# Kernel optimization log

Measured on AMD Instinct MI355X. Metric: run time of the kernel, lower is better.

Reference implementation:

```python
import jax, jax.numpy as jnp
import numpy as np


def gcn_conv(h, edge_index, num_nodes):
    # Symmetric-normalized GCN aggregation: out[i] = sum_{(j->i)} h[j] / sqrt(deg(i)*deg(j))
    row, col = edge_index[0], edge_index[1]
    deg = jax.ops.segment_sum(jnp.ones(col.shape, dtype=h.dtype), col, num_segments=num_nodes)
    d_inv_sqrt = jnp.where(deg > 0, jax.lax.rsqrt(jnp.maximum(deg, 1.0)), 0.0)
    w = d_inv_sqrt[row] * d_inv_sqrt[col]           # [E]
    msg = h[row] * w[:, None]                        # [E, D] gather + scale
    return jax.ops.segment_sum(msg, col, num_segments=num_nodes)  # [N, D] scatter-add


def setup_inputs() -> dict:
    key = jax.random.key(0)
    k1, k2, k3, k4 = jax.random.split(key, 4)
    N, E, F_IN, F_HID, F_OUT = 100000, 1600000, 128, 64, 40
    x = jax.random.normal(k1, (N, F_IN), dtype=jnp.float32)
    edge_index = jax.random.randint(k2, (2, E), 0, N, dtype=jnp.int64)
    # xavier_uniform with gain=1.414 (as in reset_parameters); biases zero
    def xavier(k, shape, gain=1.414):
        fan_out, fan_in = shape
        a = gain * np.sqrt(6.0 / (fan_in + fan_out))
        return jax.random.uniform(k, shape, jnp.float32, -a, a)
    W1 = xavier(k3, (F_HID, F_IN))
    b1 = jnp.zeros((F_HID,), dtype=jnp.float32)
    W2 = xavier(k4, (F_OUT, F_HID))
    b2 = jnp.zeros((F_OUT,), dtype=jnp.float32)
    return {"x": x, "edge_index": edge_index, "W1": W1, "b1": b1, "W2": W2, "b2": b2}


def reference(x, edge_index, W1, b1, W2, b2):
    # GNN.forward with num_layers=2, use_mp=True, eval mode (dropout inactive)
    N = x.shape[0]
    h = x @ W1.T                      # [N, nhid]
    h = gcn_conv(h, edge_index, N)
    h = jax.nn.relu(h + b1)
    h = h @ W2.T                      # [N, nclass]
    h = gcn_conv(h, edge_index, N)
    return h + b2
```

## Files before the change

kernel.cpp:

```cpp
#include <hip/hip_runtime.h>
#include <hip/hip_fp16.h>


typedef __attribute__((ext_vector_type(8))) _Float16 half8v;
typedef __attribute__((ext_vector_type(4))) float   float4v;

__device__ __forceinline__ void binfill_body(char* smem, const int* __restrict__ ed,
                                             int* __restrict__ gbincnt,
                                             unsigned* __restrict__ binbuf,
                                             int E, int cap, int bid) {
  int*            hist   = (int*)smem;
  int*            cursor = hist + 512;
  unsigned*       rec    = (unsigned*)(cursor + 512);
  unsigned short* binv   = (unsigned short*)(rec + 4096);
  int*            s_is64 = (int*)(binv + 4096);
  int t = threadIdx.x;
  hist[t] = 0; hist[t + 256] = 0;
  if (t == 0) *s_is64 = 1;
  __syncthreads();
  {
    int any = 0;
    #pragma unroll
    for (int u = 0; u < 8; ++u) {
      int idx = 2 * (t * 8 + u) + 1;
      if (idx < 2 * E && ed[idx] != 0) any = 1;
    }
    if (any) *s_is64 = 0;
  }
  __syncthreads();
  const int is64 = *s_is64;
  const int base = bid * 4096;
  const int nE = min(4096, E - base);
  for (int j = t; j < nE; j += 256) {
    int e = base + j;
    int r = is64 ? ed[2 * e] : ed[e];
    int c = is64 ? ed[2 * (E + e)] : ed[E + e];
    rec[j] = (unsigned)r | ((unsigned)(c & 255) << 17);
    binv[j] = (unsigned short)(c >> 8);
    atomicAdd(&hist[c >> 8], 1);
  }
  __syncthreads();
  for (int b = t; b < 512; b += 256) {
    int h = hist[b];
    cursor[b] = h ? atomicAdd(&gbincnt[b], h) : 0;
  }
  __syncthreads();
  for (int j = t; j < nE; j += 256) {
    int bin = binv[j];
    int pos = atomicAdd(&cursor[bin], 1);
    if (pos < cap)
      binbuf[(size_t)bin * cap + pos] = rec[j];
  }
}

__device__ __forceinline__ void gemm1_body(char* smem, const float* __restrict__ X,
                                           const float* __restrict__ W,
                                           unsigned char* __restrict__ h1q,
                                           float* __restrict__ sc1, int N, int bid) {
  _Float16* wl = (_Float16*)smem;
  const int t = threadIdx.x;
  const int row0 = bid * 128;
  const int w = t >> 6, l = t & 63;
  const int m0 = w * 32;
  const int lr = l & 15, q = l >> 4;

  float4 xr[4][2][2];
  #pragma unroll
  for (int kc = 0; kc < 4; ++kc) {
    #pragma unroll
    for (int mt = 0; mt < 2; ++mt) {
      int row = min(row0 + m0 + mt * 16 + lr, N - 1);
      const float* p = &X[(size_t)row * 128 + kc * 32 + q * 8];
      xr[kc][mt][0] = *(const float4*)p;
      xr[kc][mt][1] = *(const float4*)(p + 4);
    }
  }

  #pragma unroll
  for (int j = 0; j < 8; ++j) {
    int qq = t + 256 * j;
    int r = qq >> 5, k4 = qq & 31;
    float4 v = *(const float4*)&W[(size_t)r * 128 + k4 * 4];
    _Float16 h4[4] = {(_Float16)v.x, (_Float16)v.y, (_Float16)v.z, (_Float16)v.w};
    int k = (k4 * 4) ^ ((r & 7) * 8);
    *(float2*)&wl[r * 128 + k] = *(float2*)h4;
  }
  __syncthreads();

  float4v acc[2][4] = {};
  #pragma unroll
  for (int kc = 0; kc < 4; ++kc) {
    half8v a[2], b[4];
    #pragma unroll
    for (int mt = 0; mt < 2; ++mt) {
      float4 v0 = xr[kc][mt][0], v1 = xr[kc][mt][1];
      _Float16 h8[8] = {(_Float16)v0.x, (_Float16)v0.y, (_Float16)v0.z, (_Float16)v0.w,
                        (_Float16)v1.x, (_Float16)v1.y, (_Float16)v1.z, (_Float16)v1.w};
      a[mt] = *(half8v*)h8;
    }
    #pragma unroll
    for (int nt = 0; nt < 4; ++nt) {
      int n = nt * 16 + lr;
      int k = (kc * 32 + q * 8) ^ ((n & 7) * 8);
      b[nt] = *(half8v*)&wl[n * 128 + k];
    }
    #pragma unroll
    for (int mt = 0; mt < 2; ++mt)
      #pragma unroll
      for (int nt = 0; nt < 4; ++nt)
        acc[mt][nt] = __builtin_amdgcn_mfma_f32_16x16x32_f16(a[mt], b[nt], acc[mt][nt], 0, 0, 0);
  }

  #pragma unroll
  for (int mt = 0; mt < 2; ++mt) {
    #pragma unroll
    for (int r = 0; r < 4; ++r) {
      int row = row0 + m0 + mt * 16 + q * 4 + r;
      if (row < N) {
        float v0 = acc[mt][0][r];
        float v1 = acc[mt][1][r];
        float v2 = acc[mt][2][r];
        float v3 = acc[mt][3][r];
        float m = fmaxf(fmaxf(fabsf(v0), fabsf(v1)), fmaxf(fabsf(v2), fabsf(v3)));
        #pragma unroll
        for (int off = 1; off < 16; off <<= 1)
          m = fmaxf(m, __shfl_xor(m, off));
        float inv = (m > 0.f) ? (127.f / m) : 0.f;
        unsigned char* dst = h1q + (size_t)row * 64;
        int q0 = (int)rintf(v0 * inv);
        int q1 = (int)rintf(v1 * inv);
        int q2 = (int)rintf(v2 * inv);
        int q3 = (int)rintf(v3 * inv);
        q0 = max(-127, min(127, q0));
        q1 = max(-127, min(127, q1));
        q2 = max(-127, min(127, q2));
        q3 = max(-127, min(127, q3));
        dst[lr]      = (unsigned char)(signed char)q0;
        dst[lr + 16] = (unsigned char)(signed char)q1;
        dst[lr + 32] = (unsigned char)(signed char)q2;
        dst[lr + 48] = (unsigned char)(signed char)q3;
        if (lr == 0) sc1[row] = m * (1.f / 127.f);
      }
    }
  }
}

__launch_bounds__(256)
__global__ void k_prep(const int* __restrict__ ed, int* __restrict__ gbincnt,
                       unsigned* __restrict__ binbuf, int E, int cap,
                       const float* __restrict__ X, const float* __restrict__ W,
                       unsigned char* __restrict__ h1q, float* __restrict__ sc1,
                       int N, int FB) {
  __shared__ __align__(16) char smem[28680];
  if (blockIdx.x < FB)
    binfill_body(smem, ed, gbincnt, binbuf, E, cap, blockIdx.x);
  else
    gemm1_body(smem, X, W, h1q, sc1, N, blockIdx.x - FB);
}

__global__ void k_degscat(const unsigned* __restrict__ binbuf, const int* __restrict__ gbincnt,
                          float* __restrict__ dis, int* __restrict__ rowptr,
                          int* __restrict__ srcs, float* __restrict__ sc1,
                          int NBINS, int N, int cap) {
  __shared__ int sd[512];
  __shared__ int cnt[256];
  __shared__ int sc[256];
  __shared__ int bc[256][8];
  __shared__ unsigned rec[8192];
  int t = threadIdx.x, b = blockIdx.x;
  sd[t]       = (t < NBINS)       ? min(gbincnt[t], cap)       : 0;
  sd[t + 256] = (t + 256 < NBINS) ? min(gbincnt[t + 256], cap) : 0;
  cnt[t] = 0;
  #pragma unroll
  for (int k = 0; k < 8; ++k) bc[t][k] = 0;
  __syncthreads();
  for (int off = 1; off < 512; off <<= 1) {
    int v0 = (t >= off) ? sd[t - off] : 0;
    int v1 = sd[t + 256 - off];
    __syncthreads();
    sd[t] += v0; sd[t + 256] += v1;
    __syncthreads();
  }
  const int mybase = (b == 0) ? 0 : sd[b - 1];
  if (b == NBINS - 1 && t == 0) rowptr[N] = sd[NBINS - 1];

  int n = min(gbincnt[b], cap);
  const unsigned* buf = binbuf + (size_t)b * cap;
  for (int j = t; j < n; j += 256) {
    unsigned v = buf[j];
    rec[j] = v;
    atomicAdd(&cnt[v >> 17], 1);
    atomicAdd(&bc[v >> 17][(v & 0x1FFFF) >> 14], 1);
  }
  __syncthreads();
  sc[t] = cnt[t];
  __syncthreads();
  for (int off = 1; off < 256; off <<= 1) {
    int v = (t >= off) ? sc[t - off] : 0;
    __syncthreads();
    sc[t] += v;
    __syncthreads();
  }
  int rp = mybase + ((t == 0) ? 0 : sc[t - 1]);
  int node = b * 256 + t;
  if (node < N) {
    int d = cnt[t];
    float dv = (d > 0) ? rsqrtf((float)d) : 0.f;
    dis[node] = dv;
    rowptr[node] = rp;
    sc1[node] *= dv;
  }
  {
    int base2 = rp;
    #pragma unroll
    for (int k = 0; k < 8; ++k) {
      int c = bc[t][k];
      bc[t][k] = base2;
      base2 += c;
    }
  }
  __syncthreads();
  for (int j = t; j < n; j += 256) {
    unsigned v = rec[j];
    int pos = atomicAdd(&bc[v >> 17][(v & 0x1FFFF) >> 14], 1);
    srcs[pos] = (int)(v & 0x1FFFF);
  }
}

__launch_bounds__(256)
__global__ void k_gemm2_mfma(const __half* __restrict__ Xh, const float* __restrict__ W,
                             const float* __restrict__ dis, unsigned char* __restrict__ h2,
                             int N) {
  __shared__ _Float16 xl[128 * 64];
  __shared__ _Float16 wl[48 * 64];
  const int t = threadIdx.x;
  const int row0 = blockIdx.x * 128;

  for (int i = t; i < 48 * 8; i += 256) {
    int c = i >> 3, kq = i & 7;
    _Float16 h8[8];
    #pragma unroll
    for (int j = 0; j < 8; ++j)
      h8[j] = (c < 40) ? (_Float16)W[c * 64 + kq * 8 + j] : (_Float16)0.f;
    *(float4*)&wl[c * 64 + ((kq * 8) ^ ((c & 7) * 8))] = *(float4*)h8;
  }
  for (int i = t; i < 1024; i += 256) {
    int r = i >> 3, kq = i & 7;
    int row = row0 + r;
    float4 v = make_float4(0.f, 0.f, 0.f, 0.f);
    if (row < N) v = *(const float4*)&Xh[(size_t)row * 64 + kq * 8];
    *(float4*)&xl[r * 64 + ((kq * 8) ^ ((r & 7) * 8))] = v;
  }
  __syncthreads();

  const int w = t >> 6, l = t & 63;
  const int m0 = w * 32;
  const int lr = l & 15, q = l >> 4;

  float4v acc[2][3] = {};
  #pragma unroll
  for (int kc = 0; kc < 2; ++kc) {
    half8v a[2], b[3];
    #pragma unroll
    for (int mt = 0; mt < 2; ++mt) {
      int m = m0 + mt * 16 + lr;
      int k = (kc * 32 + q * 8) ^ ((m & 7) * 8);
      a[mt] = *(half8v*)&xl[m * 64 + k];
    }
    #pragma unroll
    for (int nt = 0; nt < 3; ++nt) {
      int n = nt * 16 + lr;
      int k = (kc * 32 + q * 8) ^ ((n & 7) * 8);
      b[nt] = *(half8v*)&wl[n * 64 + k];
    }
    #pragma unroll
    for (int mt = 0; mt < 2; ++mt)
      #pragma unroll
      for (int nt = 0; nt < 3; ++nt)
        acc[mt][nt] = __builtin_amdgcn_mfma_f32_16x16x32_f16(a[mt], b[nt], acc[mt][nt], 0, 0, 0);
  }

  #pragma unroll
  for (int mt = 0; mt < 2; ++mt) {
    #pragma unroll
    for (int r = 0; r < 4; ++r) {
      int row = row0 + m0 + mt * 16 + q * 4 + r;
      if (row < N) {
        float dr = dis[row];
        float v0 = acc[mt][0][r] * dr;
        float v1 = acc[mt][1][r] * dr;
        float v2 = acc[mt][2][r] * dr;
        float m = fmaxf(fabsf(v0), fmaxf(fabsf(v1), fabsf(v2)));
        #pragma unroll
        for (int off = 1; off < 16; off <<= 1)
          m = fmaxf(m, __shfl_xor(m, off));
        float s = m * (1.f / 127.f);
        float inv = (m > 0.f) ? (127.f / m) : 0.f;
        unsigned char* dst = h2 + (size_t)row * 64;
        int q0 = (int)rintf(v0 * inv);
        int q1 = (int)rintf(v1 * inv);
        int q2 = (int)rintf(v2 * inv);
        q0 = max(-127, min(127, q0));
        q1 = max(-127, min(127, q1));
        q2 = max(-127, min(127, q2));
        dst[lr]      = (unsigned char)(signed char)q0;
        dst[lr + 16] = (unsigned char)(signed char)q1;
        if (lr + 32 < 40) dst[lr + 32] = (unsigned char)(signed char)q2;
        if (lr == 0) *(float*)&dst[40] = s;
        if (lr >= 1 && lr <= 5) *(int*)&dst[40 + 4 * lr] = 0;
      }
    }
  }
}

__launch_bounds__(256)
__global__ void k_conv64(const unsigned char* __restrict__ H, const float* __restrict__ sc1,
                         const int* __restrict__ rowptr, const int* __restrict__ srcs,
                         const float* __restrict__ dis, const float* __restrict__ b1,
                         __half* __restrict__ out, int N) {
  int t = threadIdx.x;
  int li = t & 7;
  int node = blockIdx.x * 32 + (t >> 3);
  if (node >= N) return;
  int s = rowptr[node], e = rowptr[node + 1];
  int last = e - 1;
  float a0 = 0.f, a1 = 0.f, a2 = 0.f, a3 = 0.f,
        a4 = 0.f, a5 = 0.f, a6 = 0.f, a7 = 0.f;
  for (int p = s; p < e; p += 8) {
    int sv[8]; uint2 rv[8]; float cv[8];
    #pragma unroll
    for (int u = 0; u < 8; ++u) sv[u] = srcs[min(p + u, last)];
    #pragma unroll
    for (int u = 0; u < 8; ++u) rv[u] = *(const uint2*)&H[(size_t)sv[u] * 64 + 8 * li];
    #pragma unroll
    for (int u = 0; u < 8; ++u) cv[u] = sc1[sv[u]];
    #pragma unroll
    for (int u = 0; u < 8; ++u) {
      if (p + u < e) {
        int x0 = (int)rv[u].x, x1 = (int)rv[u].y;
        float c = cv[u];
        a0 = fmaf((float)((x0 << 24) >> 24), c, a0);
        a1 = fmaf((float)((x0 << 16) >> 24), c, a1);
        a2 = fmaf((float)((x0 << 8)  >> 24), c, a2);
        a3 = fmaf((float)( x0        >> 24), c, a3);
        a4 = fmaf((float)((x1 << 24) >> 24), c, a4);
        a5 = fmaf((float)((x1 << 16) >> 24), c, a5);
        a6 = fmaf((float)((x1 << 8)  >> 24), c, a6);
        a7 = fmaf((float)( x1        >> 24), c, a7);
      }
    }
  }
  float dn = dis[node];
  const float* bb = b1 + 8 * li;
  __half hv[8];
  hv[0] = __float2half_rn(fmaxf(fmaf(a0, dn, bb[0]), 0.f));
  hv[1] = __float2half_rn(fmaxf(fmaf(a1, dn, bb[1]), 0.f));
  hv[2] = __float2half_rn(fmaxf(fmaf(a2, dn, bb[2]), 0.f));
  hv[3] = __float2half_rn(fmaxf(fmaf(a3, dn, bb[3]), 0.f));
  hv[4] = __float2half_rn(fmaxf(fmaf(a4, dn, bb[4]), 0.f));
  hv[5] = __float2half_rn(fmaxf(fmaf(a5, dn, bb[5]), 0.f));
  hv[6] = __float2half_rn(fmaxf(fmaf(a6, dn, bb[6]), 0.f));
  hv[7] = __float2half_rn(fmaxf(fmaf(a7, dn, bb[7]), 0.f));
  *(float4*)&out[(size_t)node * 64 + 8 * li] = *(float4*)hv;
}

__launch_bounds__(256)
__global__ void k_conv40(const unsigned char* __restrict__ H, const int* __restrict__ rowptr,
                         const int* __restrict__ srcs, const float* __restrict__ dis,
                         const float* __restrict__ b2, float* __restrict__ out, int N) {
  int t = threadIdx.x;
  int li = t & 7;
  int node = blockIdx.x * 32 + (t >> 3);
  if (node >= N) return;
  bool act = li < 5;
  int s = rowptr[node], e = rowptr[node + 1];
  int last = e - 1;
  float a0 = 0.f, a1 = 0.f, a2 = 0.f, a3 = 0.f,
        a4 = 0.f, a5 = 0.f, a6 = 0.f, a7 = 0.f;
  for (int p = s; p < e; p += 8) {
    int sv[8];
    #pragma unroll
    for (int u = 0; u < 8; ++u) sv[u] = srcs[min(p + u, last)];
    if (act) {
      uint2 rv[8]; float cv[8];
      #pragma unroll
      for (int u = 0; u < 8; ++u)
        rv[u] = *(const uint2*)&H[(size_t)sv[u] * 64 + 8 * li];
      #pragma unroll
      for (int u = 0; u < 8; ++u)
        cv[u] = *(const float*)&H[(size_t)sv[u] * 64 + 40];
      #pragma unroll
      for (int u = 0; u < 8; ++u) {
        if (p + u < e) {
          int x0 = (int)rv[u].x, x1 = (int)rv[u].y;
          float c = cv[u];
          a0 = fmaf((float)((x0 << 24) >> 24), c, a0);
          a1 = fmaf((float)((x0 << 16) >> 24), c, a1);
          a2 = fmaf((float)((x0 << 8)  >> 24), c, a2);
          a3 = fmaf((float)( x0        >> 24), c, a3);
          a4 = fmaf((float)((x1 << 24) >> 24), c, a4);
          a5 = fmaf((float)((x1 << 16) >> 24), c, a5);
          a6 = fmaf((float)((x1 << 8)  >> 24), c, a6);
          a7 = fmaf((float)( x1        >> 24), c, a7);
        }
      }
    }
  }
  if (act) {
    float dn = dis[node];
    const float* bb = b2 + 8 * li;
    float4 v0 = make_float4(fmaf(a0, dn, bb[0]), fmaf(a1, dn, bb[1]),
                            fmaf(a2, dn, bb[2]), fmaf(a3, dn, bb[3]));
    float4 v1 = make_float4(fmaf(a4, dn, bb[4]), fmaf(a5, dn, bb[5]),
                            fmaf(a6, dn, bb[6]), fmaf(a7, dn, bb[7]));
    *(float4*)&out[(size_t)node * 40 + 8 * li] = v0;
    *(float4*)&out[(size_t)node * 40 + 8 * li + 4] = v1;
  }
}

extern "C" void kernel_launch(void* const* d_in, const int* in_sizes, int n_in,
                              void* d_out, int out_size, void* d_ws, size_t ws_size,
                              hipStream_t stream) {
  const float* x  = (const float*)d_in[0];
  const int*   ed = (const int*)d_in[1];
  const float* W1 = (const float*)d_in[2];
  const float* b1 = (const float*)d_in[3];
  const float* W2 = (const float*)d_in[4];
  const float* b2 = (const float*)d_in[5];
  float* out = (float*)d_out;

  const int FIN = 128, FH = 64;
  const int N = in_sizes[0] / FIN;
  const int E = in_sizes[1] / 2;
  const int NBINS = (N + 255) >> 8;
  const int cap = 8192;

  char* ws = (char*)d_ws;
  size_t off = 0;
  auto alloc = [&](size_t bytes) {
    void* p = ws + off;
    off = (off + bytes + 255) & ~(size_t)255;
    return p;
  };
  int*           gbincnt = (int*)alloc(512 * 4);
  float*         dis     = (float*)alloc((size_t)N * 4);
  int*           rowptr  = (int*)alloc(((size_t)N + 1) * 4);
  int*           srcs    = (int*)alloc((size_t)E * 4);
  unsigned*      binbuf  = (unsigned*)alloc((size_t)NBINS * cap * 4);
  unsigned char* h1q     = (unsigned char*)alloc((size_t)N * 64);
  float*         sc1     = (float*)alloc((size_t)N * 4);
  __half*        h1b     = (__half*)alloc((size_t)N * FH * 2);
  unsigned char* h2      = (unsigned char*)alloc((size_t)N * 64);

  hipMemsetAsync(gbincnt, 0, 512 * 4, stream);

  int fb = (E + 4095) / 4096;
  int mb = (N + 127) / 128;
  int cb = (N + 31) / 32;
  k_prep<<<fb + mb, 256, 0, stream>>>(ed, gbincnt, binbuf, E, cap, x, W1, h1q, sc1, N, fb);
  k_degscat<<<NBINS, 256, 0, stream>>>(binbuf, gbincnt, dis, rowptr, srcs, sc1,
                                       NBINS, N, cap);
  k_conv64<<<cb, 256, 0, stream>>>(h1q, sc1, rowptr, srcs, dis, b1, h1b, N);
  k_gemm2_mfma<<<mb, 256, 0, stream>>>(h1b, W2, dis, h2, N);
  k_conv40<<<cb, 256, 0, stream>>>(h2, rowptr, srcs, dis, b2, out, N);
}
```

Before: 210.6 us.

## Fuse first-layer aggregation with second GEMM and halve binning chunk size

The layer-1 aggregation kernel and the layer-2 MFMA GEMM are merged into one kernel. Each block aggregates 32 nodes, writes the ReLU'd fp16 rows into LDS and multiplies them by W2 in place, so the fp16 intermediate h1b no longer goes through global memory and one launch disappears. Edge binning now uses 2048-edge chunks instead of 4096, with smaller shared memory, to get more blocks and more occupancy. Risks: only half the waves do MFMA work, every block reloads W2, and the smaller k_prep shared buffer must still be big enough for the GEMM1 path.

```diff
diff --git a/kernel.cpp b/kernel.cpp
--- a/kernel.cpp
+++ b/kernel.cpp
@@ -12,8 +12,8 @@
   int*            hist   = (int*)smem;
   int*            cursor = hist + 512;
   unsigned*       rec    = (unsigned*)(cursor + 512);
-  unsigned short* binv   = (unsigned short*)(rec + 4096);
-  int*            s_is64 = (int*)(binv + 4096);
+  unsigned short* binv   = (unsigned short*)(rec + 2048);
+  int*            s_is64 = (int*)(binv + 2048);
   int t = threadIdx.x;
   hist[t] = 0; hist[t + 256] = 0;
   if (t == 0) *s_is64 = 1;
@@ -29,8 +29,8 @@
   }
   __syncthreads();
   const int is64 = *s_is64;
-  const int base = bid * 4096;
-  const int nE = min(4096, E - base);
+  const int base = bid * 2048;
+  const int nE = min(2048, E - base);
   for (int j = t; j < nE; j += 256) {
     int e = base + j;
     int r = is64 ? ed[2 * e] : ed[e];
@@ -151,7 +151,7 @@
                        const float* __restrict__ X, const float* __restrict__ W,
                        unsigned char* __restrict__ h1q, float* __restrict__ sc1,
                        int N, int FB) {
-  __shared__ __align__(16) char smem[28680];
+  __shared__ __align__(16) char smem[16512];
   if (blockIdx.x < FB)
     binfill_body(smem, ed, gbincnt, binbuf, E, cap, blockIdx.x);
   else
@@ -228,68 +228,101 @@
 }
 
 __launch_bounds__(256)
-__global__ void k_gemm2_mfma(const __half* __restrict__ Xh, const float* __restrict__ W,
-                             const float* __restrict__ dis, unsigned char* __restrict__ h2,
-                             int N) {
-  __shared__ _Float16 xl[128 * 64];
+__global__ void k_conv64g2(const unsigned char* __restrict__ H, const float* __restrict__ sc1,
+                           const int* __restrict__ rowptr, const int* __restrict__ srcs,
+                           const float* __restrict__ dis, const float* __restrict__ b1,
+                           const float* __restrict__ W2, unsigned char* __restrict__ h2,
+                           int N) {
+  __shared__ _Float16 xl[32 * 64];
   __shared__ _Float16 wl[48 * 64];
-  const int t = threadIdx.x;
-  const int row0 = blockIdx.x * 128;
+  int t = threadIdx.x;
 
   for (int i = t; i < 48 * 8; i += 256) {
     int c = i >> 3, kq = i & 7;
-    _Float16 h8[8];
+    _Float16 h8w[8];
     #pragma unroll
     for (int j = 0; j < 8; ++j)
-      h8[j] = (c < 40) ? (_Float16)W[c * 64 + kq * 8 + j] : (_Float16)0.f;
-    *(float4*)&wl[c * 64 + ((kq * 8) ^ ((c & 7) * 8))] = *(float4*)h8;
-  }
-  for (int i = t; i < 1024; i += 256) {
-    int r = i >> 3, kq = i & 7;
-    int row = row0 + r;
-    float4 v = make_float4(0.f, 0.f, 0.f, 0.f);
-    if (row < N) v = *(const float4*)&Xh[(size_t)row * 64 + kq * 8];
-    *(float4*)&xl[r * 64 + ((kq * 8) ^ ((r & 7) * 8))] = v;
-  }
-  __syncthreads();
-
-  const int w = t >> 6, l = t & 63;
-  const int m0 = w * 32;
-  const int lr = l & 15, q = l >> 4;
-
-  float4v acc[2][3] = {};
-  #pragma unroll
-  for (int kc = 0; kc < 2; ++kc) {
-    half8v a[2], b[3];
-    #pragma unroll
-    for (int mt = 0; mt < 2; ++mt) {
-      int m = m0 + mt * 16 + lr;
-      int k = (kc * 32 + q * 8) ^ ((m & 7) * 8);
-      a[mt] = *(half8v*)&xl[m * 64 + k];
-    }
-    #pragma unroll
-    for (int nt = 0; nt < 3; ++nt) {
-      int n = nt * 16 + lr;
-      int k = (kc * 32 + q * 8) ^ ((n & 7) * 8);
-      b[nt] = *(half8v*)&wl[n * 64 + k];
-    }
-    #pragma unroll
-    for (int mt = 0; mt < 2; ++mt)
-      #pragma unroll
-      for (int nt = 0; nt < 3; ++nt)
-        acc[mt][nt] = __builtin_amdgcn_mfma_f32_16x16x32_f16(a[mt], b[nt], acc[mt][nt], 0, 0, 0);
-  }
-
-  #pragma unroll
-  for (int mt = 0; mt < 2; ++mt) {
-    #pragma unroll
-    for (int r = 0; r < 4; ++r) {
-      int row = row0 + m0 + mt * 16 + q * 4 + r;
+      h8w[j] = (c < 40) ? (_Float16)W2[c * 64 + kq * 8 + j] : (_Float16)0.f;
+    *(float4*)&wl[c * 64 + ((kq * 8) ^ ((c & 7) * 8))] = *(float4*)h8w;
+  }
+
+  int li = t & 7;
+  int r = t >> 3;
+  int node = blockIdx.x * 32 + r;
+  float a0 = 0.f, a1 = 0.f, a2 = 0.f, a3 = 0.f,
+        a4 = 0.f, a5 = 0.f, a6 = 0.f, a7 = 0.f;
+  if (node < N) {
+    int s = rowptr[node], e = rowptr[node + 1];
+    int last = e - 1;
+    for (int p = s; p < e; p += 8) {
+      int sv[8]; uint2 rv[8]; float cv[8];
+      #pragma unroll
+      for (int u = 0; u < 8; ++u) sv[u] = srcs[min(p + u, last)];
+      #pragma unroll
+      for (int u = 0; u < 8; ++u) rv[u] = *(const uint2*)&H[(size_t)sv[u] * 64 + 8 * li];
+      #pragma unroll
+      for (int u = 0; u < 8; ++u) cv[u] = sc1[sv[u]];
+      #pragma unroll
+      for (int u = 0; u < 8; ++u) {
+        if (p + u < e) {
+          int x0 = (int)rv[u].x, x1 = (int)rv[u].y;
+          float c = cv[u];
+          a0 = fmaf((float)((x0 << 24) >> 24), c, a0);
+          a1 = fmaf((float)((x0 << 16) >> 24), c, a1);
+          a2 = fmaf((float)((x0 << 8)  >> 24), c, a2);
+          a3 = fmaf((float)( x0        >> 24), c, a3);
+          a4 = fmaf((float)((x1 << 24) >> 24), c, a4);
+          a5 = fmaf((float)((x1 << 16) >> 24), c, a5);
+          a6 = fmaf((float)((x1 << 8)  >> 24), c, a6);
+          a7 = fmaf((float)( x1        >> 24), c, a7);
+        }
+      }
+    }
+  }
+  {
+    _Float16 h8[8] = {};
+    if (node < N) {
+      float dn = dis[node];
+      const float* bb = b1 + 8 * li;
+      h8[0] = (_Float16)fmaxf(fmaf(a0, dn, bb[0]), 0.f);
+      h8[1] = (_Float16)fmaxf(fmaf(a1, dn, bb[1]), 0.f);
+      h8[2] = (_Float16)fmaxf(fmaf(a2, dn, bb[2]), 0.f);
+      h8[3] = (_Float16)fmaxf(fmaf(a3, dn, bb[3]), 0.f);
+      h8[4] = (_Float16)fmaxf(fmaf(a4, dn, bb[4]), 0.f);
+      h8[5] = (_Float16)fmaxf(fmaf(a5, dn, bb[5]), 0.f);
+      h8[6] = (_Float16)fmaxf(fmaf(a6, dn, bb[6]), 0.f);
+      h8[7] = (_Float16)fmaxf(fmaf(a7, dn, bb[7]), 0.f);
+    }
+    *(float4*)&xl[r * 64 + ((li * 8) ^ ((r & 7) * 8))] = *(float4*)h8;
+  }
+  __syncthreads();
+
+  int w = t >> 6, l = t & 63;
+  if ((w & 1) == 0) {
+    int tile = w >> 1;
+    int lr = l & 15, q = l >> 4;
+    float4v acc[3] = {};
+    #pragma unroll
+    for (int kc = 0; kc < 2; ++kc) {
+      int m = tile * 16 + lr;
+      int ka = (kc * 32 + q * 8) ^ ((m & 7) * 8);
+      half8v a = *(half8v*)&xl[m * 64 + ka];
+      #pragma unroll
+      for (int nt = 0; nt < 3; ++nt) {
+        int n = nt * 16 + lr;
+        int kb = (kc * 32 + q * 8) ^ ((n & 7) * 8);
+        half8v bfr = *(half8v*)&wl[n * 64 + kb];
+        acc[nt] = __builtin_amdgcn_mfma_f32_16x16x32_f16(a, bfr, acc[nt], 0, 0, 0);
+      }
+    }
+    #pragma unroll
+    for (int r2 = 0; r2 < 4; ++r2) {
+      int row = blockIdx.x * 32 + tile * 16 + q * 4 + r2;
       if (row < N) {
         float dr = dis[row];
-        float v0 = acc[mt][0][r] * dr;
-        float v1 = acc[mt][1][r] * dr;
-        float v2 = acc[mt][2][r] * dr;
+        float v0 = acc[0][r2] * dr;
+        float v1 = acc[1][r2] * dr;
+        float v2 = acc[2][r2] * dr;
         float m = fmaxf(fabsf(v0), fmaxf(fabsf(v1), fabsf(v2)));
         #pragma unroll
         for (int off = 1; off < 16; off <<= 1)
@@ -314,57 +347,6 @@
 }
 
 __launch_bounds__(256)
-__global__ void k_conv64(const unsigned char* __restrict__ H, const float* __restrict__ sc1,
-                         const int* __restrict__ rowptr, const int* __restrict__ srcs,
-                         const float* __restrict__ dis, const float* __restrict__ b1,
-                         __half* __restrict__ out, int N) {
-  int t = threadIdx.x;
-  int li = t & 7;
-  int node = blockIdx.x * 32 + (t >> 3);
-  if (node >= N) return;
-  int s = rowptr[node], e = rowptr[node + 1];
-  int last = e - 1;
-  float a0 = 0.f, a1 = 0.f, a2 = 0.f, a3 = 0.f,
-        a4 = 0.f, a5 = 0.f, a6 = 0.f, a7 = 0.f;
-  for (int p = s; p < e; p += 8) {
-    int sv[8]; uint2 rv[8]; float cv[8];
-    #pragma unroll
-    for (int u = 0; u < 8; ++u) sv[u] = srcs[min(p + u, last)];
-    #pragma unroll
-    for (int u = 0; u < 8; ++u) rv[u] = *(const uint2*)&H[(size_t)sv[u] * 64 + 8 * li];
-    #pragma unroll
-    for (int u = 0; u < 8; ++u) cv[u] = sc1[sv[u]];
-    #pragma unroll
-    for (int u = 0; u < 8; ++u) {
-      if (p + u < e) {
-        int x0 = (int)rv[u].x, x1 = (int)rv[u].y;
-        float c = cv[u];
-        a0 = fmaf((float)((x0 << 24) >> 24), c, a0);
-        a1 = fmaf((float)((x0 << 16) >> 24), c, a1);
-        a2 = fmaf((float)((x0 << 8)  >> 24), c, a2);
-        a3 = fmaf((float)( x0        >> 24), c, a3);
-        a4 = fmaf((float)((x1 << 24) >> 24), c, a4);
-        a5 = fmaf((float)((x1 << 16) >> 24), c, a5);
-        a6 = fmaf((float)((x1 << 8)  >> 24), c, a6);
-        a7 = fmaf((float)( x1        >> 24), c, a7);
-      }
-    }
-  }
-  float dn = dis[node];
-  const float* bb = b1 + 8 * li;
-  __half hv[8];
-  hv[0] = __float2half_rn(fmaxf(fmaf(a0, dn, bb[0]), 0.f));
-  hv[1] = __float2half_rn(fmaxf(fmaf(a1, dn, bb[1]), 0.f));
-  hv[2] = __float2half_rn(fmaxf(fmaf(a2, dn, bb[2]), 0.f));
-  hv[3] = __float2half_rn(fmaxf(fmaf(a3, dn, bb[3]), 0.f));
-  hv[4] = __float2half_rn(fmaxf(fmaf(a4, dn, bb[4]), 0.f));
-  hv[5] = __float2half_rn(fmaxf(fmaf(a5, dn, bb[5]), 0.f));
-  hv[6] = __float2half_rn(fmaxf(fmaf(a6, dn, bb[6]), 0.f));
-  hv[7] = __float2half_rn(fmaxf(fmaf(a7, dn, bb[7]), 0.f));
-  *(float4*)&out[(size_t)node * 64 + 8 * li] = *(float4*)hv;
-}
-
-__launch_bounds__(256)
 __global__ void k_conv40(const unsigned char* __restrict__ H, const int* __restrict__ rowptr,
                          const int* __restrict__ srcs, const float* __restrict__ dis,
                          const float* __restrict__ b2, float* __restrict__ out, int N) {
@@ -429,7 +411,7 @@
   const float* b2 = (const float*)d_in[5];
   float* out = (float*)d_out;
 
-  const int FIN = 128, FH = 64;
+  const int FIN = 128;
   const int N = in_sizes[0] / FIN;
   const int E = in_sizes[1] / 2;
   const int NBINS = (N + 255) >> 8;
@@ -449,18 +431,16 @@
   unsigned*      binbuf  = (unsigned*)alloc((size_t)NBINS * cap * 4);
   unsigned char* h1q     = (unsigned char*)alloc((size_t)N * 64);
   float*         sc1     = (float*)alloc((size_t)N * 4);
-  __half*        h1b     = (__half*)alloc((size_t)N * FH * 2);
   unsigned char* h2      = (unsigned char*)alloc((size_t)N * 64);
 
   hipMemsetAsync(gbincnt, 0, 512 * 4, stream);
 
-  int fb = (E + 4095) / 4096;
+  int fb = (E + 2047) / 2048;
   int mb = (N + 127) / 128;
   int cb = (N + 31) / 32;
   k_prep<<<fb + mb, 256, 0, stream>>>(ed, gbincnt, binbuf, E, cap, x, W1, h1q, sc1, N, fb);
   k_degscat<<<NBINS, 256, 0, stream>>>(binbuf, gbincnt, dis, rowptr, srcs, sc1,
                                        NBINS, N, cap);
-  k_conv64<<<cb, 256, 0, stream>>>(h1q, sc1, rowptr, srcs, dis, b1, h1b, N);
-  k_gemm2_mfma<<<mb, 256, 0, stream>>>(h1b, W2, dis, h2, N);
+  k_conv64g2<<<cb, 256, 0, stream>>>(h1q, sc1, rowptr, srcs, dis, b1, W2, h2, N);
   k_conv40<<<cb, 256, 0, stream>>>(h2, rowptr, srcs, dis, b2, out, N);
 }
```

New measurement: 229.6 us. 1.09x slower.
